# Kernel optimization log

Measured on AMD Instinct MI355X. Metric: run time of the kernel, lower is better.

## Reference

```python
import jax, jax.numpy as jnp
import numpy as np

NV, NF, DIM = 6144, 12288, 256


def _linear(x, W, b):
    # torch nn.Linear: x @ W.T + b, W has shape (out, in)
    return x @ W.T + b


def _agg(X, A, Wf, bf, Wg, bg):
    # AGG: out_fc = Linear(A @ X); out_gagg = Linear(A @ out_fc)  (eval mode: dropout is identity)
    out_fc = _linear(A @ X, Wf, bf)
    out_g = _linear(A @ out_fc, Wg, bg)
    return jax.nn.relu(out_fc + out_g)


def setup_inputs() -> dict:
    key = jax.random.key(0)
    ks = jax.random.split(key, 18)
    primal = jax.random.normal(ks[0], (NV, DIM), jnp.float32)
    # degree-normalized adjacency (docstring): scale uniform entries by 1/N for stable row sums
    A_primal = jax.random.uniform(ks[1], (NV, NV), jnp.float32) * (1.0 / NV)
    A_dual = jax.random.uniform(ks[2], (NF, NF), jnp.float32) * (1.0 / NF)
    A = jax.random.uniform(ks[3], (NV, NF), jnp.float32) * (1.0 / NF)
    faces = jax.random.randint(ks[4], (NF, 3), 0, NV)

    w = lambda k, shp: jax.random.normal(k, shp, jnp.float32) * 0.05
    return {
        "primal": primal, "A_primal": A_primal, "A_dual": A_dual, "A": A, "faces": faces,
        # 3 primal AGG layers (fc + gagg), stacked on leading axis
        "pW": w(ks[5], (3, DIM, DIM)), "pb": w(ks[6], (3, DIM)),
        "pgW": w(ks[7], (3, DIM, DIM)), "pgb": w(ks[8], (3, DIM)),
        # 3 dual AGG layers
        "dW": w(ks[9], (3, DIM, DIM)), "db": w(ks[10], (3, DIM)),
        "dgW": w(ks[11], (3, DIM, DIM)), "dgb": w(ks[12], (3, DIM)),
        # PDF linears: (dim, 2*dim)
        "Wp": w(ks[13], (DIM, 2 * DIM)), "bp": w(ks[14], (DIM,)),
        "Wd": w(ks[15], (DIM, 2 * DIM)), "bd": w(ks[16], (DIM,)),
    }


def reference(primal, A_primal, A_dual, A, faces, pW, pb, pgW, pgb, dW, db, dgW, dgb, Wp, bp, Wd, bd):
    x_p = primal
    x_d = (1.0 / 3.0) * (A.T @ primal)  # primal_dual
    primal_outs, dual_outs = [], []
    for i in range(3):
        primal_outs.append(x_p)
        x_p = _agg(x_p, A_primal, pW[i], pb[i], pgW[i], pgb[i]) + x_p
    for i in range(3):
        dual_outs.append(x_d)
        x_d = _agg(x_d, A_dual, dW[i], db[i], dgW[i], dgb[i]) + x_d
    # PDF: DAP gather-reduce  (N_f, 3, dim) -> (N_f, dim)
    f = jnp.mean(jnp.abs(x_p[faces] - x_d[:, None, :]), axis=1)
    out_dual = jax.nn.relu(_linear(jnp.concatenate([x_d, f], axis=1), Wd, bd))
    mapped = A @ f  # dual_primal
    out_primal = jax.nn.relu(_linear(jnp.concatenate([x_p, mapped], axis=1), Wp, bp))
    return (out_primal + x_p, out_dual + x_d, *primal_outs, *dual_outs)
```

## Files before the change

### kernel.cpp

```cpp
#include <hip/hip_runtime.h>


typedef short short8 __attribute__((ext_vector_type(8)));
typedef float floatx4 __attribute__((ext_vector_type(4)));
typedef unsigned short ushort4v __attribute__((ext_vector_type(4)));
typedef unsigned short u16;

#define DIMN 256
#define GBK 64

static const int kNV = 6144;
static const int kNF = 12288;
static const int SLAB = 768;

__device__ __forceinline__ float bf2f(u16 u) {
  union { unsigned int i; float f; } x; x.i = ((unsigned int)u) << 16; return x.f;
}
__device__ __forceinline__ u16 f2bf(float f) {
  union { float f; unsigned int i; } x; x.f = f;
  unsigned int r = x.i + 0x7fffu + ((x.i >> 16) & 1u);
  return (u16)(r >> 16);
}
__device__ __forceinline__ void gld_lds16(const void* g, void* l) {
  __builtin_amdgcn_global_load_lds((__attribute__((address_space(1))) void*)(g),
                                   (__attribute__((address_space(3))) void*)(l),
                                   16, 0, 0);
}

__global__ __launch_bounds__(256, 2)
void gemm_bf16_k(const void* __restrict__ A0, int A0mode, int lda0,
                 const void* __restrict__ A1, int A1mode, int lda1, int K1,
                 const void* __restrict__ Bt, int Btis32, int ldb,
                 u16* __restrict__ P, int M, int nx, int kchunk,
                 int fused, const float* __restrict__ bias,
                 const u16* __restrict__ addmat, int do_relu,
                 const float* __restrict__ resid,
                 float* __restrict__ outf, u16* __restrict__ out16,
                 u16* __restrict__ outT)
{
  __shared__ __align__(16) u16 As[2][128 * GBK];
  __shared__ __align__(16) u16 Bs[2][128 * GBK];

  const int d = blockIdx.x;
  const int y = d & 1;
  const int bx = (d >> 1) % nx;
  const int bz = (d >> 1) / nx;
  const int m0 = bx << 7;
  const int n0 = y << 7;
  const int kb = bz * kchunk;
  const int nkt = kchunk / GBK;

  const int tid = threadIdx.x;
  const int wid = tid >> 6;
  const int lane = tid & 63;
  const int wr = wid >> 1, wc = wid & 1;
  const int srow = lane >> 3;
  const int skk = (lane & 7) << 3;

  floatx4 acc[4][4];
  floatx4 zz = {0.f, 0.f, 0.f, 0.f};
#pragma unroll
  for (int i = 0; i < 4; ++i)
#pragma unroll
    for (int j = 0; j < 4; ++j) acc[i][j] = zz;

  auto stage = [&](int buf, int k0) {
    const void* base; int lda, mode, kl;
    if (k0 < K1) { base = A0; lda = lda0; mode = A0mode; kl = k0; }
    else         { base = A1; lda = lda1; mode = A1mode; kl = k0 - K1; }
    if (mode == 0) {
      const u16* U = (const u16*)base;
#pragma unroll
      for (int j = 0; j < 4; ++j) {
        int c = (wid << 2) + j;
        gld_lds16(U + (size_t)(m0 + (c << 3) + srow) * lda + kl + skk,
                  (void*)&As[buf][c << 9]);
      }
    } else {
      const float* F = (const float*)base;
#pragma unroll
      for (int j = 0; j < 4; ++j) {
        int c = (wid << 2) + j;
        const size_t gi = (size_t)(m0 + (c << 3) + srow) * lda + kl + skk;
        floatx4 f0 = *(const floatx4*)(F + gi);
        floatx4 f1 = *(const floatx4*)(F + gi + 4);
        short8 v;
#pragma unroll
        for (int e = 0; e < 4; ++e) { v[e] = (short)f2bf(f0[e]); v[4 + e] = (short)f2bf(f1[e]); }
        *(short8*)&As[buf][(c << 9) + (lane << 3)] = v;
      }
    }
    if (Btis32) {
      const float* F = (const float*)Bt;
#pragma unroll
      for (int j = 0; j < 4; ++j) {
        int c = (wid << 2) + j;
        const size_t gi = (size_t)(n0 + (c << 3) + srow) * ldb + k0 + skk;
        floatx4 f0 = *(const floatx4*)(F + gi);
        floatx4 f1 = *(const floatx4*)(F + gi + 4);
        short8 v;
#pragma unroll
        for (int e = 0; e < 4; ++e) { v[e] = (short)f2bf(f0[e]); v[4 + e] = (short)f2bf(f1[e]); }
        *(short8*)&Bs[buf][(c << 9) + (lane << 3)] = v;
      }
    } else {
      const u16* U = (const u16*)Bt;
#pragma unroll
      for (int j = 0; j < 4; ++j) {
        int c = (wid << 2) + j;
        gld_lds16(U + (size_t)(n0 + (c << 3) + srow) * ldb + k0 + skk,
                  (void*)&Bs[buf][c << 9]);
      }
    }
  };

  int cur = 0;
  stage(0, kb);
  for (int kt = 0; kt < nkt; ++kt) {
    __syncthreads();
    if (kt + 1 < nkt) stage(cur ^ 1, kb + (kt + 1) * GBK);
#pragma unroll
    for (int ks = 0; ks < 2; ++ks) {
      short8 a[4], b[4];
      const int ko = (ks << 5) + ((lane >> 4) << 3);
#pragma unroll
      for (int mi = 0; mi < 4; ++mi)
        a[mi] = *(const short8*)&As[cur][((wr << 6) + (mi << 4) + (lane & 15)) * GBK + ko];
#pragma unroll
      for (int ni = 0; ni < 4; ++ni)
        b[ni] = *(const short8*)&Bs[cur][((wc << 6) + (ni << 4) + (lane & 15)) * GBK + ko];
#pragma unroll
      for (int mi = 0; mi < 4; ++mi)
#pragma unroll
        for (int ni = 0; ni < 4; ++ni)
          acc[mi][ni] = __builtin_amdgcn_mfma_f32_16x16x32_bf16(a[mi], b[ni], acc[mi][ni], 0, 0, 0);
    }
    cur ^= 1;
  }

  if (fused) {
    u16* ts = (u16*)&As[0][0];
    if (outT) __syncthreads();
#pragma unroll
    for (int mi = 0; mi < 4; ++mi) {
#pragma unroll
      for (int ni = 0; ni < 4; ++ni) {
        const int ml0 = (wr << 6) + (mi << 4) + ((lane >> 4) << 2);
        const int nl = (wc << 6) + (ni << 4) + (lane & 15);
        const int n = n0 + nl;
        const float bv = bias ? bias[n] : 0.f;
#pragma unroll
        for (int r = 0; r < 4; ++r) {
          const int ml = ml0 + r;
          const size_t idx = (size_t)(m0 + ml) * DIMN + n;
          float t = acc[mi][ni][r] + bv;
          if (addmat) t += bf2f(addmat[idx]);
          if (do_relu) t = fmaxf(t, 0.f);
          if (resid) t += resid[idx];
          if (outf) outf[idx] = t;
          const u16 q = f2bf(t);
          if (out16) out16[idx] = q;
          if (outT) ts[ml * 128 + (nl ^ ((ml & 7) << 3))] = q;
        }
      }
    }
    if (outT) {
      __syncthreads();
      const int nl = tid >> 1;
      const int mh = (tid & 1) << 6;
#pragma unroll
      for (int c8 = 0; c8 < 8; ++c8) {
        const int mB = mh + (c8 << 3);
        short8 v;
#pragma unroll
        for (int e = 0; e < 8; ++e)
          v[e] = (short)ts[(mB + e) * 128 + (nl ^ (((mB + e) & 7) << 3))];
        *(short8*)&outT[(size_t)(n0 + nl) * M + (m0 + mB)] = v;
      }
    }
  } else {
    u16* Pz = P + (size_t)bz * (size_t)M * DIMN;
#pragma unroll
    for (int mi = 0; mi < 4; ++mi) {
#pragma unroll
      for (int ni = 0; ni < 4; ++ni) {
        const int mb = m0 + (wr << 6) + (mi << 4) + ((lane >> 4) << 2);
        const int n = n0 + (wc << 6) + (ni << 4) + (lane & 15);
#pragma unroll
        for (int r = 0; r < 4; ++r)
          Pz[(size_t)(mb + r) * DIMN + n] = f2bf(acc[mi][ni][r]);
      }
    }
  }
}

__global__ __launch_bounds__(256)
void finalize_k(const u16* __restrict__ P, int S, int Mrows, float scale,
                float* __restrict__ out, u16* __restrict__ out16)
{
  const size_t MN = (size_t)Mrows * DIMN;
  const size_t i4 = (((size_t)blockIdx.x * blockDim.x) + threadIdx.x) * 4;
  if (i4 >= MN) return;
  floatx4 v = {0.f, 0.f, 0.f, 0.f};
  for (int s = 0; s < S; ++s) {
    ushort4v p4 = *(const ushort4v*)(P + (size_t)s * MN + i4);
#pragma unroll
    for (int j = 0; j < 4; ++j) v[j] += bf2f(p4[j]);
  }
  floatx4 o;
#pragma unroll
  for (int j = 0; j < 4; ++j) o[j] = v[j] * scale;
  if (out) *(floatx4*)(out + i4) = o;
  if (out16) {
    unsigned long long q = 0;
#pragma unroll
    for (int j = 0; j < 4; ++j) q |= ((unsigned long long)f2bf(o[j])) << (16 * j);
    *(unsigned long long*)(out16 + i4) = q;
  }
}

__global__ __launch_bounds__(256)
void finalize_tr_k(const u16* __restrict__ P, int S, int Mrows, float scale,
                   float* __restrict__ outf, u16* __restrict__ outT, int ldT)
{
  __shared__ __align__(16) u16 t[64][64];
  const size_t MN = (size_t)Mrows * DIMN;
  const int r0 = blockIdx.x << 6;
  const int c0 = blockIdx.y << 6;
  const int tid = threadIdx.x;
  const int lr = tid >> 3;
  const int lc = (tid & 7) << 3;
#pragma unroll
  for (int h = 0; h < 2; ++h) {
    const int r = lr + (h << 5);
    const size_t gi = (size_t)(r0 + r) * DIMN + (c0 + lc);
    float a[8];
#pragma unroll
    for (int e = 0; e < 8; ++e) a[e] = 0.f;
    for (int s = 0; s < S; ++s) {
      short8 p = *(const short8*)(P + (size_t)s * MN + gi);
#pragma unroll
      for (int e = 0; e < 8; ++e) a[e] += bf2f((u16)p[e]);
    }
    short8 v;
    floatx4 o0, o1;
#pragma unroll
    for (int e = 0; e < 4; ++e) {
      o0[e] = a[e] * scale; o1[e] = a[4 + e] * scale;
      v[e] = (short)f2bf(o0[e]); v[4 + e] = (short)f2bf(o1[e]);
    }
    *(floatx4*)(outf + gi) = o0;
    *(floatx4*)(outf + gi + 4) = o1;
    *(short8*)&t[r][lc ^ ((r >> 3) << 3)] = v;
  }
  __syncthreads();
#pragma unroll
  for (int h = 0; h < 2; ++h) {
    const int oc = lr + (h << 5);
    short8 v;
#pragma unroll
    for (int e = 0; e < 8; ++e)
      v[e] = (short)t[lc + e][oc ^ ((lc >> 3) << 3)];
    *(short8*)&outT[(size_t)(c0 + oc) * ldT + (r0 + lc)] = v;
  }
}

__global__ __launch_bounds__(256)
void transpose_k(const void* __restrict__ in, int is32, int ldin,
                 u16* __restrict__ out, int ldout, u16* __restrict__ copy16)
{
  __shared__ __align__(16) u16 t[64][64];
  const int c0 = blockIdx.x << 6;
  const int r0 = blockIdx.y << 6;
  const int tid = threadIdx.x;
  const int lr = tid >> 3;
  const int lc = (tid & 7) << 3;
#pragma unroll
  for (int h = 0; h < 2; ++h) {
    const int r = lr + (h << 5);
    short8 v;
    if (is32) {
      const float* F = (const float*)in;
      const size_t gi = (size_t)(r0 + r) * ldin + (c0 + lc);
      floatx4 f0 = *(const floatx4*)(F + gi);
      floatx4 f1 = *(const floatx4*)(F + gi + 4);
#pragma unroll
      for (int e = 0; e < 4; ++e) { v[e] = (short)f2bf(f0[e]); v[4 + e] = (short)f2bf(f1[e]); }
      if (copy16) *(short8*)(copy16 + gi) = v;
    } else {
      v = *(const short8*)((const u16*)in + (size_t)(r0 + r) * ldin + (c0 + lc));
    }
    *(short8*)&t[r][lc ^ ((r >> 3) << 3)] = v;
  }
  __syncthreads();
#pragma unroll
  for (int h = 0; h < 2; ++h) {
    const int oc = lr + (h << 5);
    short8 v;
#pragma unroll
    for (int e = 0; e < 8; ++e)
      v[e] = (short)t[lc + e][oc ^ ((lc >> 3) << 3)];
    *(short8*)&out[(size_t)(c0 + oc) * ldout + (r0 + lc)] = v;
  }
}

__global__ __launch_bounds__(256)
void cvt8_k(const float* __restrict__ in, u16* __restrict__ out, size_t n)
{
  const size_t stride = (size_t)gridDim.x * 2048;
  for (size_t i = (((size_t)blockIdx.x << 8) + threadIdx.x) << 3; i < n; i += stride) {
    floatx4 f0 = *(const floatx4*)(in + i);
    floatx4 f1 = *(const floatx4*)(in + i + 4);
    short8 v;
#pragma unroll
    for (int e = 0; e < 4; ++e) { v[e] = (short)f2bf(f0[e]); v[4 + e] = (short)f2bf(f1[e]); }
    *(short8*)(out + i) = v;
  }
}

__global__ __launch_bounds__(256)
void face_gather_k(const float* __restrict__ xp, const float* __restrict__ xd,
                   const int* __restrict__ faces, u16* __restrict__ f)
{
  const int fi = blockIdx.x;
  const int j = threadIdx.x;
  const int a = faces[fi * 3 + 0];
  const int b = faces[fi * 3 + 1];
  const int c = faces[fi * 3 + 2];
  const float xv = xd[(size_t)fi * DIMN + j];
  const float s = fabsf(xp[(size_t)a * DIMN + j] - xv)
                + fabsf(xp[(size_t)b * DIMN + j] - xv)
                + fabsf(xp[(size_t)c * DIMN + j] - xv);
  f[(size_t)fi * DIMN + j] = f2bf(s * (1.0f / 3.0f));
}

extern "C" void kernel_launch(void* const* d_in, const int* in_sizes, int n_in,
                              void* d_out, int out_size, void* d_ws, size_t ws_size,
                              hipStream_t stream)
{
  (void)in_sizes; (void)n_in; (void)out_size;
  const float* primal   = (const float*)d_in[0];
  const float* A_primal = (const float*)d_in[1];
  const float* A_dual   = (const float*)d_in[2];
  const float* A        = (const float*)d_in[3];
  const int* faces      = (const int*)d_in[4];
  const float* pW  = (const float*)d_in[5];
  const float* pb  = (const float*)d_in[6];
  const float* pgW = (const float*)d_in[7];
  const float* pgb = (const float*)d_in[8];
  const float* dW  = (const float*)d_in[9];
  const float* db  = (const float*)d_in[10];
  const float* dgW = (const float*)d_in[11];
  const float* dgb = (const float*)d_in[12];
  const float* Wp  = (const float*)d_in[13];
  const float* bp  = (const float*)d_in[14];
  const float* Wd  = (const float*)d_in[15];
  const float* bd  = (const float*)d_in[16];

  char* wsp = (char*)d_ws;
  auto alloc = [&](size_t bytes) -> void* {
    void* p = (void*)wsp;
    wsp += (bytes + 255) & ~(size_t)255;
    return p;
  };
  const size_t NVD = (size_t)kNV * DIMN, NFD = (size_t)kNF * DIMN;
  u16* XTp   = (u16*)alloc(NVD * 2);
  u16* XTd   = (u16*)alloc(NFD * 2);
  u16* TB    = (u16*)alloc(NFD * 2);
  u16* t1    = (u16*)alloc(NFD * 2);
  u16* fc    = (u16*)alloc(NFD * 2);
  float* xp3 = (float*)alloc(NVD * 4);
  float* xd3 = (float*)alloc(NFD * 4);
  u16* P     = (u16*)alloc((size_t)8 * NFD * 2);
  const size_t bigElems = (size_t)kNF * kNF + 2 * (size_t)kNF * kNV + (size_t)kNV * kNV;
  const size_t need = (size_t)(wsp - (char*)d_ws) + bigElems * 2 + 4096;
  const bool big = ws_size >= need;
  u16 *Ad16 = nullptr, *At16 = nullptr, *A16 = nullptr, *Ap16 = nullptr;
  if (big) {
    Ad16 = (u16*)alloc((size_t)kNF * kNF * 2);
    At16 = (u16*)alloc((size_t)kNF * kNV * 2);
    A16  = (u16*)alloc((size_t)kNV * kNF * 2);
    Ap16 = (u16*)alloc((size_t)kNV * kNV * 2);
  }

  float* out0  = (float*)d_out;
  float* out1  = out0 + NVD;
  float* pouts = out1 + NFD;
  float* douts = pouts + 3 * NVD;

  auto gemmP = [&](const void* A0p, int a0mode, int lda0,
                   const u16* Btp, int ldb, int M, int K, int S) {
    const int nx = M / 128;
    gemm_bf16_k<<<dim3(nx * 2 * S), dim3(256), 0, stream>>>(
        A0p, a0mode, lda0, nullptr, 0, 0, K, Btp, 0, ldb,
        P, M, nx, K / S, 0, nullptr, nullptr, 0, nullptr, nullptr, nullptr, nullptr);
  };
  auto gemmF = [&](const void* A0p, int a0mode, int lda0,
                   const void* A1p, int a1mode, int lda1, int K1,
                   const void* Btp, int btis32, int ldb, int M, int K,
                   const float* bias, const u16* add, int relu,
                   const float* resid, float* outf, u16* out16, u16* outT) {
    const int nx = M / 128;
    gemm_bf16_k<<<dim3(nx * 2), dim3(256), 0, stream>>>(
        A0p, a0mode, lda0, A1p, a1mode, lda1, K1, Btp, btis32, ldb,
        P, M, nx, K, 1, bias, add, relu, resid, outf, out16, outT);
  };
  auto fin = [&](int M, int S, float scale, float* out, u16* out16) {
    finalize_k<<<dim3((unsigned)((size_t)M * DIMN / 1024)), dim3(256), 0, stream>>>(
        P, S, M, scale, out, out16);
  };
  auto tranp = [&](const void* in, int is32, int ldin, u16* out, int ldout,
                   int R, int C, u16* copy16) {
    transpose_k<<<dim3(C / 64, R / 64), dim3(256), 0, stream>>>(
        in, is32, ldin, out, ldout, copy16);
  };
  auto cvt = [&](const float* in, u16* out, size_t n) {
    cvt8_k<<<dim3(2048), dim3(256), 0, stream>>>(in, out, n);
  };

  if (big) {
    cvt(A_dual, Ad16, (size_t)kNF * kNF);
    cvt(A_primal, Ap16, (size_t)kNV * kNV);
    tranp(A, 1, kNF, At16, kNV, kNV, kNF, A16);
  }
  tranp(primal, 1, DIMN, XTp, kNV, kNV, DIMN, nullptr);
  hipMemcpyAsync(pouts, primal, NVD * 4, hipMemcpyDeviceToDevice, stream);

  if (big) {
    gemmP(At16, 0, kNV, XTp, kNV, kNF, kNV, 4);
    finalize_tr_k<<<dim3(kNF / 64, 4), dim3(256), 0, stream>>>(
        P, 4, kNF, 1.0f / 3.0f, douts, XTd, kNF);
  } else {
    for (int s = 0; s < kNF / SLAB; ++s) {
      const int m0 = s * SLAB;
      tranp(A + m0, 1, kNF, TB, kNV, kNV, SLAB, nullptr);
      gemmP(TB, 0, kNV, XTp, kNV, SLAB, kNV, 16);
      finalize_k<<<dim3((unsigned)((size_t)SLAB * DIMN / 1024)), dim3(256), 0, stream>>>(
          P, 16, SLAB, 1.0f / 3.0f, douts + (size_t)m0 * DIMN, nullptr);
    }
    tranp(douts, 1, DIMN, XTd, kNF, kNF, DIMN, nullptr);
  }

  const void* ApP = big ? (const void*)Ap16 : (const void*)A_primal;
  const int apm = big ? 0 : 1;
  const void* AdP = big ? (const void*)Ad16 : (const void*)A_dual;
  const int adm = big ? 0 : 1;

  const float* xpc = primal;
  for (int i = 0; i < 3; ++i) {
    gemmP(ApP, apm, kNV, XTp, kNV, kNV, kNV, 8);
    fin(kNV, 8, 1.f, nullptr, t1);
    gemmF(t1, 0, 256, nullptr, 0, 0, 256,
          pW + (size_t)i * 65536, 1, 256, kNV, 256,
          pb + i * 256, nullptr, 0, nullptr, nullptr, fc, TB);
    gemmP(ApP, apm, kNV, TB, kNV, kNV, kNV, 8);
    fin(kNV, 8, 1.f, nullptr, t1);
    float* nxt = (i < 2) ? (pouts + (size_t)(i + 1) * NVD) : xp3;
    u16* xtT = (i < 2) ? XTp : nullptr;
    gemmF(t1, 0, 256, nullptr, 0, 0, 256,
          pgW + (size_t)i * 65536, 1, 256, kNV, 256,
          pgb + i * 256, fc, 1, xpc, nxt, nullptr, xtT);
    xpc = nxt;
  }

  const float* xdc = douts;
  for (int i = 0; i < 3; ++i) {
    gemmP(AdP, adm, kNF, XTd, kNF, kNF, kNF, 4);
    fin(kNF, 4, 1.f, nullptr, t1);
    gemmF(t1, 0, 256, nullptr, 0, 0, 256,
          dW + (size_t)i * 65536, 1, 256, kNF, 256,
          db + i * 256, nullptr, 0, nullptr, nullptr, fc, TB);
    gemmP(AdP, adm, kNF, TB, kNF, kNF, kNF, 4);
    fin(kNF, 4, 1.f, nullptr, t1);
    float* nxt = (i < 2) ? (douts + (size_t)(i + 1) * NFD) : xd3;
    u16* xtT = (i < 2) ? XTd : nullptr;
    gemmF(t1, 0, 256, nullptr, 0, 0, 256,
          dgW + (size_t)i * 65536, 1, 256, kNF, 256,
          dgb + i * 256, fc, 1, xdc, nxt, nullptr, xtT);
    xdc = nxt;
  }

  face_gather_k<<<dim3(kNF), dim3(256), 0, stream>>>(xp3, xd3, faces, t1);
  tranp(t1, 0, DIMN, TB, kNF, kNF, DIMN, nullptr);
  gemmF(xd3, 1, 256, t1, 0, 256, 256, Wd, 1, 512, kNF, 512,
        bd, nullptr, 1, xd3, out1, nullptr, nullptr);
  if (big) gemmP(A16, 0, kNF, TB, kNF, kNV, kNF, 8);
  else     gemmP(A, 1, kNF, TB, kNF, kNV, kNF, 8);
  fin(kNV, 8, 1.f, nullptr, fc);
  gemmF(xp3, 1, 256, fc, 0, 256, 256, Wp, 1, 512, kNV, 512,
        bp, nullptr, 1, xp3, out0, nullptr, nullptr);
}
```

Measured before the change: 2.132 ms.

## Add 512-thread full-width bf16 GEMM with triple-buffered LDS for adjacency products

Adds a new split-K GEMM kernel that uses 512 threads. Each block computes a 128x256 tile covering the full feature width, so each A tile is loaded once instead of twice across N halves. The kernel stages loads with a 3-slot global_load_lds pipeline and XOR-swizzled LDS, and the split-K factor is doubled to keep occupancy up. In exchange, the partial-sum buffer grows and the finalize step has more partial slices to reduce. The new kernel replaces the generic path for all big adjacency GEMMs when workspace allows.

Result: slower. 2.178 ms (+2.2%).

```diff
diff --git a/kernel.cpp b/kernel.cpp
--- a/kernel.cpp
+++ b/kernel.cpp
@@ -25,6 +25,105 @@
   __builtin_amdgcn_global_load_lds((__attribute__((address_space(1))) void*)(g),
                                    (__attribute__((address_space(3))) void*)(l),
                                    16, 0, 0);
+}
+
+__global__ __launch_bounds__(512, 1)
+void gemm8_k(const u16* __restrict__ A, int lda,
+             const u16* __restrict__ Bt, int ldb,
+             u16* __restrict__ P, int M, int nx, int kchunk)
+{
+  __shared__ __align__(16) u16 As[3][128 * 64];
+  __shared__ __align__(16) u16 Bs[3][256 * 64];
+
+  const int d = blockIdx.x;
+  const int bx = d % nx;
+  const int bz = d / nx;
+  const int m0 = bx << 7;
+  const int kb = bz * kchunk;
+  const int nkt = kchunk >> 6;
+
+  const int tid = threadIdx.x;
+  const int wid = tid >> 6, lane = tid & 63;
+  const int wr = wid >> 2, wc = wid & 3;
+  const int srow = lane >> 3;
+  const int scol = ((lane & 7) ^ srow) << 3;
+
+  floatx4 acc[4][4];
+  floatx4 zz = {0.f, 0.f, 0.f, 0.f};
+#pragma unroll
+  for (int i = 0; i < 4; ++i)
+#pragma unroll
+    for (int j = 0; j < 4; ++j) acc[i][j] = zz;
+
+  auto stage = [&](int slot, int k0) {
+#pragma unroll
+    for (int j = 0; j < 2; ++j) {
+      int c = (wid << 1) + j;
+      gld_lds16(A + (size_t)(m0 + (c << 3) + srow) * lda + k0 + scol,
+                (void*)&As[slot][c << 9]);
+    }
+#pragma unroll
+    for (int j = 0; j < 4; ++j) {
+      int c = (wid << 2) + j;
+      gld_lds16(Bt + (size_t)((c << 3) + srow) * ldb + k0 + scol,
+                (void*)&Bs[slot][c << 9]);
+    }
+  };
+
+  stage(0, kb);
+  if (nkt > 1) stage(1, kb + GBK);
+
+  int cur = 0;
+  for (int t = 0; t < nkt; ++t) {
+    if (t + 2 < nkt) stage((cur + 2) % 3, kb + (t + 2) * GBK);
+    if (t + 2 < nkt)      asm volatile("s_waitcnt vmcnt(12)" ::: "memory");
+    else if (t + 1 < nkt) asm volatile("s_waitcnt vmcnt(6)" ::: "memory");
+    else                  asm volatile("s_waitcnt vmcnt(0)" ::: "memory");
+    __builtin_amdgcn_s_barrier();
+
+    short8 a[4][2], b[4][2];
+#pragma unroll
+    for (int mf = 0; mf < 4; ++mf)
+#pragma unroll
+      for (int ks = 0; ks < 2; ++ks) {
+        const int row = (wr << 6) + (mf << 4) + (lane & 15);
+        const int c8 = ((ks << 2) + (lane >> 4)) ^ (row & 7);
+        a[mf][ks] = *(const short8*)&As[cur][row * 64 + (c8 << 3)];
+      }
+#pragma unroll
+    for (int nf = 0; nf < 4; ++nf)
+#pragma unroll
+      for (int ks = 0; ks < 2; ++ks) {
+        const int row = (wc << 6) + (nf << 4) + (lane & 15);
+        const int c8 = ((ks << 2) + (lane >> 4)) ^ (row & 7);
+        b[nf][ks] = *(const short8*)&Bs[cur][row * 64 + (c8 << 3)];
+      }
+    __builtin_amdgcn_s_setprio(1);
+#pragma unroll
+    for (int ks = 0; ks < 2; ++ks)
+#pragma unroll
+      for (int mf = 0; mf < 4; ++mf)
+#pragma unroll
+        for (int nf = 0; nf < 4; ++nf)
+          acc[mf][nf] = __builtin_amdgcn_mfma_f32_16x16x32_bf16(
+              a[mf][ks], b[nf][ks], acc[mf][nf], 0, 0, 0);
+    __builtin_amdgcn_s_setprio(0);
+    __builtin_amdgcn_s_barrier();
+    cur = (cur + 1) % 3;
+  }
+
+  u16* Pz = P + (size_t)bz * (size_t)M * DIMN;
+#pragma unroll
+  for (int mf = 0; mf < 4; ++mf) {
+#pragma unroll
+    for (int nf = 0; nf < 4; ++nf) {
+      const int mb = m0 + (wr << 6) + (mf << 4) + ((lane >> 4) << 2);
+      const int n = (wc << 6) + (nf << 4) + (lane & 15);
+#pragma unroll
+      for (int r = 0; r < 4; ++r)
+        Pz[(size_t)(mb + r) * DIMN + n] = f2bf(acc[mf][nf][r]);
+    }
+  }
 }
 
 __global__ __launch_bounds__(256, 2)
@@ -388,6 +487,11 @@
   float* pouts = out1 + NFD;
   float* douts = pouts + 3 * NVD;
 
+  auto gemm8 = [&](const u16* Ap, int lda, const u16* Btp, int ldb,
+                   int M, int K, int S) {
+    const int nx = M / 128;
+    gemm8_k<<<dim3(nx * S), dim3(512), 0, stream>>>(Ap, lda, Btp, ldb, P, M, nx, K / S);
+  };
   auto gemmP = [&](const void* A0p, int a0mode, int lda0,
                    const u16* Btp, int ldb, int M, int K, int S) {
     const int nx = M / 128;
@@ -427,9 +531,9 @@
   hipMemcpyAsync(pouts, primal, NVD * 4, hipMemcpyDeviceToDevice, stream);
 
   if (big) {
-    gemmP(At16, 0, kNV, XTp, kNV, kNF, kNV, 4);
+    gemm8(At16, kNV, XTp, kNV, kNF, kNV, 8);
     finalize_tr_k<<<dim3(kNF / 64, 4), dim3(256), 0, stream>>>(
-        P, 4, kNF, 1.0f / 3.0f, douts, XTd, kNF);
+        P, 8, kNF, 1.0f / 3.0f, douts, XTd, kNF);
   } else {
     for (int s = 0; s < kNF / SLAB; ++s) {
       const int m0 = s * SLAB;
@@ -441,20 +545,17 @@
     tranp(douts, 1, DIMN, XTd, kNF, kNF, DIMN, nullptr);
   }
 
-  const void* ApP = big ? (const void*)Ap16 : (const void*)A_primal;
-  const int apm = big ? 0 : 1;
-  const void* AdP = big ? (const void*)Ad16 : (const void*)A_dual;
-  const int adm = big ? 0 : 1;
-
   const float* xpc = primal;
   for (int i = 0; i < 3; ++i) {
-    gemmP(ApP, apm, kNV, XTp, kNV, kNV, kNV, 8);
-    fin(kNV, 8, 1.f, nullptr, t1);
+    if (big) gemm8(Ap16, kNV, XTp, kNV, kNV, kNV, 16);
+    else     gemmP(A_primal, 1, kNV, XTp, kNV, kNV, kNV, 8);
+    fin(kNV, big ? 16 : 8, 1.f, nullptr, t1);
     gemmF(t1, 0, 256, nullptr, 0, 0, 256,
           pW + (size_t)i * 65536, 1, 256, kNV, 256,
           pb + i * 256, nullptr, 0, nullptr, nullptr, fc, TB);
-    gemmP(ApP, apm, kNV, TB, kNV, kNV, kNV, 8);
-    fin(kNV, 8, 1.f, nullptr, t1);
+    if (big) gemm8(Ap16, kNV, TB, kNV, kNV, kNV, 16);
+    else     gemmP(A_primal, 1, kNV, TB, kNV, kNV, kNV, 8);
+    fin(kNV, big ? 16 : 8, 1.f, nullptr, t1);
     float* nxt = (i < 2) ? (pouts + (size_t)(i + 1) * NVD) : xp3;
     u16* xtT = (i < 2) ? XTp : nullptr;
     gemmF(t1, 0, 256, nullptr, 0, 0, 256,
@@ -465,13 +566,15 @@
 
   const float* xdc = douts;
   for (int i = 0; i < 3; ++i) {
-    gemmP(AdP, adm, kNF, XTd, kNF, kNF, kNF, 4);
-    fin(kNF, 4, 1.f, nullptr, t1);
+    if (big) gemm8(Ad16, kNF, XTd, kNF, kNF, kNF, 8);
+    else     gemmP(A_dual, 1, kNF, XTd, kNF, kNF, kNF, 4);
+    fin(kNF, big ? 8 : 4, 1.f, nullptr, t1);
     gemmF(t1, 0, 256, nullptr, 0, 0, 256,
           dW + (size_t)i * 65536, 1, 256, kNF, 256,
           db + i * 256, nullptr, 0, nullptr, nullptr, fc, TB);
-    gemmP(AdP, adm, kNF, TB, kNF, kNF, kNF, 4);
-    fin(kNF, 4, 1.f, nullptr, t1);
+    if (big) gemm8(Ad16, kNF, TB, kNF, kNF, kNF, 8);
+    else     gemmP(A_dual, 1, kNF, TB, kNF, kNF, kNF, 4);
+    fin(kNF, big ? 8 : 4, 1.f, nullptr, t1);
     float* nxt = (i < 2) ? (douts + (size_t)(i + 1) * NFD) : xd3;
     u16* xtT = (i < 2) ? XTd : nullptr;
     gemmF(t1, 0, 256, nullptr, 0, 0, 256,
@@ -484,9 +587,8 @@
   tranp(t1, 0, DIMN, TB, kNF, kNF, DIMN, nullptr);
   gemmF(xd3, 1, 256, t1, 0, 256, 256, Wd, 1, 512, kNF, 512,
         bd, nullptr, 1, xd3, out1, nullptr, nullptr);
-  if (big) gemmP(A16, 0, kNF, TB, kNF, kNV, kNF, 8);
-  else     gemmP(A, 1, kNF, TB, kNF, kNV, kNF, 8);
-  fin(kNV, 8, 1.f, nullptr, fc);
+  if (big) { gemm8(A16, kNF, TB, kNF, kNV, kNF, 16); fin(kNV, 16, 1.f, nullptr, fc); }
+  else     { gemmP(A, 1, kNF, TB, kNF, kNV, kNF, 8); fin(kNV, 8, 1.f, nullptr, fc); }
   gemmF(xp3, 1, 256, fc, 0, 256, 256, Wp, 1, 512, kNV, 512,
         bp, nullptr, 1, xp3, out0, nullptr, nullptr);
 }
```

## Co-schedule independent primal and dual AGG chains in combined kernel launches

Applied to the files above, without the earlier changes.

The primal and dual layer stacks are independent, so each stage now runs both branches in a single launch. Kernel arguments are packed into structs, and the block index picks which job a block executes. Separate scratch buffers per branch and split partial-sum regions make the two jobs safe to run together. The aim is fewer launches and better fill of the GPU, since the smaller primal GEMMs alone leave many compute units idle. The cost is more scratch memory and possible load imbalance between the two jobs inside one grid.

Result: faster. 1.799 ms (-15.6%).

```diff
diff --git a/kernel.cpp b/kernel.cpp
--- a/kernel.cpp
+++ b/kernel.cpp
@@ -27,28 +27,31 @@
                                    16, 0, 0);
 }
 
-__global__ __launch_bounds__(256, 2)
-void gemm_bf16_k(const void* __restrict__ A0, int A0mode, int lda0,
-                 const void* __restrict__ A1, int A1mode, int lda1, int K1,
-                 const void* __restrict__ Bt, int Btis32, int ldb,
-                 u16* __restrict__ P, int M, int nx, int kchunk,
-                 int fused, const float* __restrict__ bias,
-                 const u16* __restrict__ addmat, int do_relu,
-                 const float* __restrict__ resid,
-                 float* __restrict__ outf, u16* __restrict__ out16,
-                 u16* __restrict__ outT)
+struct GJ {
+  const void* A0; int A0mode; int lda0;
+  const void* A1; int A1mode; int lda1; int K1;
+  const void* Bt; int Btis32; int ldb;
+  u16* P; int M; int nx; int kchunk;
+  int fused;
+  const float* bias; const u16* addmat; int do_relu;
+  const float* resid; float* outf; u16* out16; u16* outT;
+};
+struct FJ {
+  const u16* P; int S; int Mrows; float scale; float* out; u16* out16;
+};
+
+__device__ __forceinline__ void gemm_dev(const GJ& j, int bid)
 {
   __shared__ __align__(16) u16 As[2][128 * GBK];
   __shared__ __align__(16) u16 Bs[2][128 * GBK];
 
-  const int d = blockIdx.x;
-  const int y = d & 1;
-  const int bx = (d >> 1) % nx;
-  const int bz = (d >> 1) / nx;
+  const int y = bid & 1;
+  const int bx = (bid >> 1) % j.nx;
+  const int bz = (bid >> 1) / j.nx;
   const int m0 = bx << 7;
   const int n0 = y << 7;
-  const int kb = bz * kchunk;
-  const int nkt = kchunk / GBK;
+  const int kb = bz * j.kchunk;
+  const int nkt = j.kchunk / GBK;
 
   const int tid = threadIdx.x;
   const int wid = tid >> 6;
@@ -62,25 +65,25 @@
 #pragma unroll
   for (int i = 0; i < 4; ++i)
 #pragma unroll
-    for (int j = 0; j < 4; ++j) acc[i][j] = zz;
+    for (int jj = 0; jj < 4; ++jj) acc[i][jj] = zz;
 
   auto stage = [&](int buf, int k0) {
     const void* base; int lda, mode, kl;
-    if (k0 < K1) { base = A0; lda = lda0; mode = A0mode; kl = k0; }
-    else         { base = A1; lda = lda1; mode = A1mode; kl = k0 - K1; }
+    if (k0 < j.K1) { base = j.A0; lda = j.lda0; mode = j.A0mode; kl = k0; }
+    else           { base = j.A1; lda = j.lda1; mode = j.A1mode; kl = k0 - j.K1; }
     if (mode == 0) {
       const u16* U = (const u16*)base;
 #pragma unroll
-      for (int j = 0; j < 4; ++j) {
-        int c = (wid << 2) + j;
+      for (int q = 0; q < 4; ++q) {
+        int c = (wid << 2) + q;
         gld_lds16(U + (size_t)(m0 + (c << 3) + srow) * lda + kl + skk,
                   (void*)&As[buf][c << 9]);
       }
     } else {
       const float* F = (const float*)base;
 #pragma unroll
-      for (int j = 0; j < 4; ++j) {
-        int c = (wid << 2) + j;
+      for (int q = 0; q < 4; ++q) {
+        int c = (wid << 2) + q;
         const size_t gi = (size_t)(m0 + (c << 3) + srow) * lda + kl + skk;
         floatx4 f0 = *(const floatx4*)(F + gi);
         floatx4 f1 = *(const floatx4*)(F + gi + 4);
@@ -90,12 +93,12 @@
         *(short8*)&As[buf][(c << 9) + (lane << 3)] = v;
       }
     }
-    if (Btis32) {
-      const float* F = (const float*)Bt;
-#pragma unroll
-      for (int j = 0; j < 4; ++j) {
-        int c = (wid << 2) + j;
-        const size_t gi = (size_t)(n0 + (c << 3) + srow) * ldb + k0 + skk;
+    if (j.Btis32) {
+      const float* F = (const float*)j.Bt;
+#pragma unroll
+      for (int q = 0; q < 4; ++q) {
+        int c = (wid << 2) + q;
+        const size_t gi = (size_t)(n0 + (c << 3) + srow) * j.ldb + k0 + skk;
         floatx4 f0 = *(const floatx4*)(F + gi);
         floatx4 f1 = *(const floatx4*)(F + gi + 4);
         short8 v;
@@ -104,11 +107,11 @@
         *(short8*)&Bs[buf][(c << 9) + (lane << 3)] = v;
       }
     } else {
-      const u16* U = (const u16*)Bt;
-#pragma unroll
-      for (int j = 0; j < 4; ++j) {
-        int c = (wid << 2) + j;
-        gld_lds16(U + (size_t)(n0 + (c << 3) + srow) * ldb + k0 + skk,
+      const u16* U = (const u16*)j.Bt;
+#pragma unroll
+      for (int q = 0; q < 4; ++q) {
+        int c = (wid << 2) + q;
+        gld_lds16(U + (size_t)(n0 + (c << 3) + srow) * j.ldb + k0 + skk,
                   (void*)&Bs[buf][c << 9]);
       }
     }
@@ -138,9 +141,9 @@
     cur ^= 1;
   }
 
-  if (fused) {
+  if (j.fused) {
     u16* ts = (u16*)&As[0][0];
-    if (outT) __syncthreads();
+    if (j.outT) __syncthreads();
 #pragma unroll
     for (int mi = 0; mi < 4; ++mi) {
 #pragma unroll
@@ -148,23 +151,23 @@
         const int ml0 = (wr << 6) + (mi << 4) + ((lane >> 4) << 2);
         const int nl = (wc << 6) + (ni << 4) + (lane & 15);
         const int n = n0 + nl;
-        const float bv = bias ? bias[n] : 0.f;
+        const float bv = j.bias ? j.bias[n] : 0.f;
 #pragma unroll
         for (int r = 0; r < 4; ++r) {
           const int ml = ml0 + r;
           const size_t idx = (size_t)(m0 + ml) * DIMN + n;
           float t = acc[mi][ni][r] + bv;
-          if (addmat) t += bf2f(addmat[idx]);
-          if (do_relu) t = fmaxf(t, 0.f);
-          if (resid) t += resid[idx];
-          if (outf) outf[idx] = t;
+          if (j.addmat) t += bf2f(j.addmat[idx]);
+          if (j.do_relu) t = fmaxf(t, 0.f);
+          if (j.resid) t += j.resid[idx];
+          if (j.outf) j.outf[idx] = t;
           const u16 q = f2bf(t);
-          if (out16) out16[idx] = q;
-          if (outT) ts[ml * 128 + (nl ^ ((ml & 7) << 3))] = q;
+          if (j.out16) j.out16[idx] = q;
+          if (j.outT) ts[ml * 128 + (nl ^ ((ml & 7) << 3))] = q;
         }
       }
     }
-    if (outT) {
+    if (j.outT) {
       __syncthreads();
       const int nl = tid >> 1;
       const int mh = (tid & 1) << 6;
@@ -175,11 +178,11 @@
 #pragma unroll
         for (int e = 0; e < 8; ++e)
           v[e] = (short)ts[(mB + e) * 128 + (nl ^ (((mB + e) & 7) << 3))];
-        *(short8*)&outT[(size_t)(n0 + nl) * M + (m0 + mB)] = v;
+        *(short8*)&j.outT[(size_t)(n0 + nl) * j.M + (m0 + mB)] = v;
       }
     }
   } else {
-    u16* Pz = P + (size_t)bz * (size_t)M * DIMN;
+    u16* Pz = j.P + (size_t)bz * (size_t)j.M * DIMN;
 #pragma unroll
     for (int mi = 0; mi < 4; ++mi) {
 #pragma unroll
@@ -194,29 +197,38 @@
   }
 }
 
-__global__ __launch_bounds__(256)
-void finalize_k(const u16* __restrict__ P, int S, int Mrows, float scale,
-                float* __restrict__ out, u16* __restrict__ out16)
-{
-  const size_t MN = (size_t)Mrows * DIMN;
-  const size_t i4 = (((size_t)blockIdx.x * blockDim.x) + threadIdx.x) * 4;
+__global__ __launch_bounds__(256, 2) void gemm1_k(GJ j0) { gemm_dev(j0, blockIdx.x); }
+__global__ __launch_bounds__(256, 2) void gemm2_k(GJ j0, GJ j1, int nb0) {
+  if ((int)blockIdx.x < nb0) gemm_dev(j0, blockIdx.x);
+  else                       gemm_dev(j1, blockIdx.x - nb0);
+}
+
+__device__ __forceinline__ void fin_dev(const FJ& f, int bid)
+{
+  const size_t MN = (size_t)f.Mrows * DIMN;
+  const size_t i4 = (((size_t)bid << 8) + threadIdx.x) * 4;
   if (i4 >= MN) return;
   floatx4 v = {0.f, 0.f, 0.f, 0.f};
-  for (int s = 0; s < S; ++s) {
-    ushort4v p4 = *(const ushort4v*)(P + (size_t)s * MN + i4);
-#pragma unroll
-    for (int j = 0; j < 4; ++j) v[j] += bf2f(p4[j]);
+  for (int s = 0; s < f.S; ++s) {
+    ushort4v p4 = *(const ushort4v*)(f.P + (size_t)s * MN + i4);
+#pragma unroll
+    for (int q = 0; q < 4; ++q) v[q] += bf2f(p4[q]);
   }
   floatx4 o;
 #pragma unroll
-  for (int j = 0; j < 4; ++j) o[j] = v[j] * scale;
-  if (out) *(floatx4*)(out + i4) = o;
-  if (out16) {
-    unsigned long long q = 0;
-#pragma unroll
-    for (int j = 0; j < 4; ++j) q |= ((unsigned long long)f2bf(o[j])) << (16 * j);
-    *(unsigned long long*)(out16 + i4) = q;
-  }
+  for (int q = 0; q < 4; ++q) o[q] = v[q] * f.scale;
+  if (f.out) *(floatx4*)(f.out + i4) = o;
+  if (f.out16) {
+    unsigned long long qq = 0;
+#pragma unroll
+    for (int q = 0; q < 4; ++q) qq |= ((unsigned long long)f2bf(o[q])) << (16 * q);
+    *(unsigned long long*)(f.out16 + i4) = qq;
+  }
+}
+__global__ __launch_bounds__(256) void fin1_k(FJ f0) { fin_dev(f0, blockIdx.x); }
+__global__ __launch_bounds__(256) void fin2_k(FJ f0, FJ f1, int nb0) {
+  if ((int)blockIdx.x < nb0) fin_dev(f0, blockIdx.x);
+  else                       fin_dev(f1, blockIdx.x - nb0);
 }
 
 __global__ __launch_bounds__(256)
@@ -323,15 +335,15 @@
                    const int* __restrict__ faces, u16* __restrict__ f)
 {
   const int fi = blockIdx.x;
-  const int j = threadIdx.x;
+  const int jj = threadIdx.x;
   const int a = faces[fi * 3 + 0];
   const int b = faces[fi * 3 + 1];
   const int c = faces[fi * 3 + 2];
-  const float xv = xd[(size_t)fi * DIMN + j];
-  const float s = fabsf(xp[(size_t)a * DIMN + j] - xv)
-                + fabsf(xp[(size_t)b * DIMN + j] - xv)
-                + fabsf(xp[(size_t)c * DIMN + j] - xv);
-  f[(size_t)fi * DIMN + j] = f2bf(s * (1.0f / 3.0f));
+  const float xv = xd[(size_t)fi * DIMN + jj];
+  const float s = fabsf(xp[(size_t)a * DIMN + jj] - xv)
+                + fabsf(xp[(size_t)b * DIMN + jj] - xv)
+                + fabsf(xp[(size_t)c * DIMN + jj] - xv);
+  f[(size_t)fi * DIMN + jj] = f2bf(s * (1.0f / 3.0f));
 }
 
 extern "C" void kernel_launch(void* const* d_in, const int* in_sizes, int n_in,
@@ -366,12 +378,17 @@
   const size_t NVD = (size_t)kNV * DIMN, NFD = (size_t)kNF * DIMN;
   u16* XTp   = (u16*)alloc(NVD * 2);
   u16* XTd   = (u16*)alloc(NFD * 2);
-  u16* TB    = (u16*)alloc(NFD * 2);
-  u16* t1    = (u16*)alloc(NFD * 2);
-  u16* fc    = (u16*)alloc(NFD * 2);
+  u16* TBd   = (u16*)alloc(NFD * 2);
+  u16* TBp   = (u16*)alloc(NVD * 2);
+  u16* t1d   = (u16*)alloc(NFD * 2);
+  u16* t1p   = (u16*)alloc(NVD * 2);
+  u16* fcd   = (u16*)alloc(NFD * 2);
+  u16* fcp   = (u16*)alloc(NVD * 2);
   float* xp3 = (float*)alloc(NVD * 4);
   float* xd3 = (float*)alloc(NFD * 4);
   u16* P     = (u16*)alloc((size_t)8 * NFD * 2);
+  u16* Pd    = P;
+  u16* Pp    = P + 4 * NFD;
   const size_t bigElems = (size_t)kNF * kNF + 2 * (size_t)kNF * kNV + (size_t)kNV * kNV;
   const size_t need = (size_t)(wsp - (char*)d_ws) + bigElems * 2 + 4096;
   const bool big = ws_size >= need;
@@ -388,27 +405,46 @@
   float* pouts = out1 + NFD;
   float* douts = pouts + 3 * NVD;
 
-  auto gemmP = [&](const void* A0p, int a0mode, int lda0,
-                   const u16* Btp, int ldb, int M, int K, int S) {
-    const int nx = M / 128;
-    gemm_bf16_k<<<dim3(nx * 2 * S), dim3(256), 0, stream>>>(
-        A0p, a0mode, lda0, nullptr, 0, 0, K, Btp, 0, ldb,
-        P, M, nx, K / S, 0, nullptr, nullptr, 0, nullptr, nullptr, nullptr, nullptr);
-  };
-  auto gemmF = [&](const void* A0p, int a0mode, int lda0,
-                   const void* A1p, int a1mode, int lda1, int K1,
-                   const void* Btp, int btis32, int ldb, int M, int K,
-                   const float* bias, const u16* add, int relu,
-                   const float* resid, float* outf, u16* out16, u16* outT) {
-    const int nx = M / 128;
-    gemm_bf16_k<<<dim3(nx * 2), dim3(256), 0, stream>>>(
-        A0p, a0mode, lda0, A1p, a1mode, lda1, K1, Btp, btis32, ldb,
-        P, M, nx, K, 1, bias, add, relu, resid, outf, out16, outT);
-  };
-  auto fin = [&](int M, int S, float scale, float* out, u16* out16) {
-    finalize_k<<<dim3((unsigned)((size_t)M * DIMN / 1024)), dim3(256), 0, stream>>>(
-        P, S, M, scale, out, out16);
-  };
+  auto GP = [&](const void* A0, int mode, int lda, const u16* Bt, int ldb,
+                u16* Pr, int M, int K, int S) -> GJ {
+    GJ g{}; g.A0 = A0; g.A0mode = mode; g.lda0 = lda;
+    g.A1 = nullptr; g.A1mode = 0; g.lda1 = 0; g.K1 = K;
+    g.Bt = Bt; g.Btis32 = 0; g.ldb = ldb;
+    g.P = Pr; g.M = M; g.nx = M / 128; g.kchunk = K / S; g.fused = 0;
+    g.bias = nullptr; g.addmat = nullptr; g.do_relu = 0; g.resid = nullptr;
+    g.outf = nullptr; g.out16 = nullptr; g.outT = nullptr;
+    return g;
+  };
+  auto GF = [&](const void* A0, int a0m, int lda0, const void* A1, int a1m,
+                int lda1, int K1, const void* Bt, int bt32, int ldb, int M, int K,
+                const float* bias, const u16* add, int relu, const float* resid,
+                float* outf, u16* out16, u16* outT) -> GJ {
+    GJ g{}; g.A0 = A0; g.A0mode = a0m; g.lda0 = lda0;
+    g.A1 = A1; g.A1mode = a1m; g.lda1 = lda1; g.K1 = K1;
+    g.Bt = Bt; g.Btis32 = bt32; g.ldb = ldb;
+    g.P = P; g.M = M; g.nx = M / 128; g.kchunk = K; g.fused = 1;
+    g.bias = bias; g.addmat = add; g.do_relu = relu; g.resid = resid;
+    g.outf = outf; g.out16 = out16; g.outT = outT;
+    return g;
+  };
+  auto gblk = [&](const GJ& g) { return g.nx * 2 * (g.fused ? 1 : (g.K1 / g.kchunk)); };
+  auto launch2 = [&](const GJ& a, const GJ& b) {
+    const int nb0 = gblk(a);
+    gemm2_k<<<dim3(nb0 + gblk(b)), dim3(256), 0, stream>>>(a, b, nb0);
+  };
+  auto launch1 = [&](const GJ& a) {
+    gemm1_k<<<dim3(gblk(a)), dim3(256), 0, stream>>>(a);
+  };
+  auto FIN = [&](const u16* Pr, int S, int M, float scale, float* out, u16* out16) -> FJ {
+    FJ f{}; f.P = Pr; f.S = S; f.Mrows = M; f.scale = scale; f.out = out; f.out16 = out16;
+    return f;
+  };
+  auto fblk = [&](const FJ& f) { return (int)((size_t)f.Mrows * DIMN / 1024); };
+  auto fin2 = [&](const FJ& a, const FJ& b) {
+    const int nb0 = fblk(a);
+    fin2_k<<<dim3(nb0 + fblk(b)), dim3(256), 0, stream>>>(a, b, nb0);
+  };
+  auto fin1 = [&](const FJ& a) { fin1_k<<<dim3(fblk(a)), dim3(256), 0, stream>>>(a); };
   auto tranp = [&](const void* in, int is32, int ldin, u16* out, int ldout,
                    int R, int C, u16* copy16) {
     transpose_k<<<dim3(C / 64, R / 64), dim3(256), 0, stream>>>(
@@ -426,67 +462,59 @@
   tranp(primal, 1, DIMN, XTp, kNV, kNV, DIMN, nullptr);
   hipMemcpyAsync(pouts, primal, NVD * 4, hipMemcpyDeviceToDevice, stream);
 
-  if (big) {
-    gemmP(At16, 0, kNV, XTp, kNV, kNF, kNV, 4);
-    finalize_tr_k<<<dim3(kNF / 64, 4), dim3(256), 0, stream>>>(
-        P, 4, kNF, 1.0f / 3.0f, douts, XTd, kNF);
-  } else {
-    for (int s = 0; s < kNF / SLAB; ++s) {
-      const int m0 = s * SLAB;
-      tranp(A + m0, 1, kNF, TB, kNV, kNV, SLAB, nullptr);
-      gemmP(TB, 0, kNV, XTp, kNV, SLAB, kNV, 16);
-      finalize_k<<<dim3((unsigned)((size_t)SLAB * DIMN / 1024)), dim3(256), 0, stream>>>(
-          P, 16, SLAB, 1.0f / 3.0f, douts + (size_t)m0 * DIMN, nullptr);
-    }
-    tranp(douts, 1, DIMN, XTd, kNF, kNF, DIMN, nullptr);
-  }
-
   const void* ApP = big ? (const void*)Ap16 : (const void*)A_primal;
   const int apm = big ? 0 : 1;
   const void* AdP = big ? (const void*)Ad16 : (const void*)A_dual;
   const int adm = big ? 0 : 1;
 
+  if (big) {
+    launch1(GP(At16, 0, kNV, XTp, kNV, Pd, kNF, kNV, 4));
+    finalize_tr_k<<<dim3(kNF / 64, 4), dim3(256), 0, stream>>>(
+        Pd, 4, kNF, 1.0f / 3.0f, douts, XTd, kNF);
+  } else {
+    for (int s = 0; s < kNF / SLAB; ++s) {
+      const int m0 = s * SLAB;
+      tranp(A + m0, 1, kNF, TBd, kNV, kNV, SLAB, nullptr);
+      launch1(GP(TBd, 0, kNV, XTp, kNV, Pd, SLAB, kNV, 16));
+      fin1(FIN(Pd, 16, SLAB, 1.0f / 3.0f, douts + (size_t)m0 * DIMN, nullptr));
+    }
+    tranp(douts, 1, DIMN, XTd, kNF, kNF, DIMN, nullptr);
+  }
+
   const float* xpc = primal;
-  for (int i = 0; i < 3; ++i) {
-    gemmP(ApP, apm, kNV, XTp, kNV, kNV, kNV, 8);
-    fin(kNV, 8, 1.f, nullptr, t1);
-    gemmF(t1, 0, 256, nullptr, 0, 0, 256,
-          pW + (size_t)i * 65536, 1, 256, kNV, 256,
-          pb + i * 256, nullptr, 0, nullptr, nullptr, fc, TB);
-    gemmP(ApP, apm, kNV, TB, kNV, kNV, kNV, 8);
-    fin(kNV, 8, 1.f, nullptr, t1);
-    float* nxt = (i < 2) ? (pouts + (size_t)(i + 1) * NVD) : xp3;
-    u16* xtT = (i < 2) ? XTp : nullptr;
-    gemmF(t1, 0, 256, nullptr, 0, 0, 256,
-          pgW + (size_t)i * 65536, 1, 256, kNV, 256,
-          pgb + i * 256, fc, 1, xpc, nxt, nullptr, xtT);
-    xpc = nxt;
-  }
-
   const float* xdc = douts;
   for (int i = 0; i < 3; ++i) {
-    gemmP(AdP, adm, kNF, XTd, kNF, kNF, kNF, 4);
-    fin(kNF, 4, 1.f, nullptr, t1);
-    gemmF(t1, 0, 256, nullptr, 0, 0, 256,
-          dW + (size_t)i * 65536, 1, 256, kNF, 256,
-          db + i * 256, nullptr, 0, nullptr, nullptr, fc, TB);
-    gemmP(AdP, adm, kNF, TB, kNF, kNF, kNF, 4);
-    fin(kNF, 4, 1.f, nullptr, t1);
-    float* nxt = (i < 2) ? (douts + (size_t)(i + 1) * NFD) : xd3;
-    u16* xtT = (i < 2) ? XTd : nullptr;
-    gemmF(t1, 0, 256, nullptr, 0, 0, 256,
-          dgW + (size_t)i * 65536, 1, 256, kNF, 256,
-          dgb + i * 256, fc, 1, xdc, nxt, nullptr, xtT);
-    xdc = nxt;
-  }
-
-  face_gather_k<<<dim3(kNF), dim3(256), 0, stream>>>(xp3, xd3, faces, t1);
-  tranp(t1, 0, DIMN, TB, kNF, kNF, DIMN, nullptr);
-  gemmF(xd3, 1, 256, t1, 0, 256, 256, Wd, 1, 512, kNF, 512,
-        bd, nullptr, 1, xd3, out1, nullptr, nullptr);
-  if (big) gemmP(A16, 0, kNF, TB, kNF, kNV, kNF, 8);
-  else     gemmP(A, 1, kNF, TB, kNF, kNV, kNF, 8);
-  fin(kNV, 8, 1.f, nullptr, fc);
-  gemmF(xp3, 1, 256, fc, 0, 256, 256, Wp, 1, 512, kNV, 512,
-        bp, nullptr, 1, xp3, out0, nullptr, nullptr);
-}
+    launch2(GP(AdP, adm, kNF, XTd, kNF, Pd, kNF, kNF, 4),
+            GP(ApP, apm, kNV, XTp, kNV, Pp, kNV, kNV, 8));
+    fin2(FIN(Pd, 4, kNF, 1.f, nullptr, t1d), FIN(Pp, 8, kNV, 1.f, nullptr, t1p));
+    launch2(GF(t1d, 0, 256, nullptr, 0, 0, 256, dW + (size_t)i * 65536, 1, 256,
+               kNF, 256, db + i * 256, nullptr, 0, nullptr, nullptr, fcd, TBd),
+            GF(t1p, 0, 256, nullptr, 0, 0, 256, pW + (size_t)i * 65536, 1, 256,
+               kNV, 256, pb + i * 256, nullptr, 0, nullptr, nullptr, fcp, TBp));
+    launch2(GP(AdP, adm, kNF, TBd, kNF, Pd, kNF, kNF, 4),
+            GP(ApP, apm, kNV, TBp, kNV, Pp, kNV, kNV, 8));
+    fin2(FIN(Pd, 4, kNF, 1.f, nullptr, t1d), FIN(Pp, 8, kNV, 1.f, nullptr, t1p));
+    float* nxd = (i < 2) ? (douts + (size_t)(i + 1) * NFD) : xd3;
+    float* nxp = (i < 2) ? (pouts + (size_t)(i + 1) * NVD) : xp3;
+    u16* xdT = (i < 2) ? XTd : nullptr;
+    u16* xpT = (i < 2) ? XTp : nullptr;
+    launch2(GF(t1d, 0, 256, nullptr, 0, 0, 256, dgW + (size_t)i * 65536, 1, 256,
+               kNF, 256, dgb + i * 256, fcd, 1, xdc, nxd, nullptr, xdT),
+            GF(t1p, 0, 256, nullptr, 0, 0, 256, pgW + (size_t)i * 65536, 1, 256,
+               kNV, 256, pgb + i * 256, fcp, 1, xpc, nxp, nullptr, xpT));
+    xdc = nxd; xpc = nxp;
+  }
+
+  face_gather_k<<<dim3(kNF), dim3(256), 0, stream>>>(xp3, xd3, faces, t1d);
+  tranp(t1d, 0, DIMN, TBd, kNF, kNF, DIMN, nullptr);
+  {
+    GJ jo = GF(xd3, 1, 256, t1d, 0, 256, 256, Wd, 1, 512, kNF, 512,
+               bd, nullptr, 1, xd3, out1, nullptr, nullptr);
+    GJ jm = big ? GP(A16, 0, kNF, TBd, kNF, Pp, kNV, kNF, 8)
+                : GP(A, 1, kNF, TBd, kNF, Pp, kNV, kNF, 8);
+    launch2(jo, jm);
+  }
+  fin1(FIN(Pp, 8, kNV, 1.f, nullptr, fcp));
+  launch1(GF(xp3, 1, 256, fcp, 0, 256, 256, Wp, 1, 512, kNV, 512,
+             bp, nullptr, 1, xp3, out0, nullptr, nullptr));
+}
```
